# Optimization experiments

Measured on AMD Instinct MI355X. Metric: run time of the kernel, lower is better.

The kernel has to match this reference:

```python
import jax, jax.numpy as jnp
import numpy as np

B, T, DMODEL = 8, 1024, 1024
N_HEADS, DK, DV = 16, 64, 64
FF_INNER = 4096


def setup_inputs() -> dict:
    key = jax.random.key(0)
    ks = jax.random.split(key, 9)
    s = 0.02  # init scale so softmax logits stay sane
    return {
        "x": jax.random.normal(ks[0], (B, T, DMODEL), dtype=jnp.float32),
        "Wq": jax.random.normal(ks[1], (N_HEADS, DMODEL, DK), dtype=jnp.float32) * s,
        "Wk": jax.random.normal(ks[2], (N_HEADS, DMODEL, DK), dtype=jnp.float32) * s,
        "Wv": jax.random.normal(ks[3], (N_HEADS, DMODEL, DV), dtype=jnp.float32) * s,
        "Wo": jax.random.normal(ks[4], (DMODEL, DMODEL), dtype=jnp.float32) * s,
        "W1": jax.random.normal(ks[5], (FF_INNER, DMODEL), dtype=jnp.float32) * s,
        "b1": jax.random.normal(ks[6], (FF_INNER,), dtype=jnp.float32) * s,
        "W2": jax.random.normal(ks[7], (DMODEL, FF_INNER), dtype=jnp.float32) * s,
        "b2": jax.random.normal(ks[8], (DMODEL,), dtype=jnp.float32) * s,
    }


def _pseudo_norm(y):
    # Original: y - mean - std (unbiased std, torch default). NOT a real layernorm.
    mean = jnp.mean(y, axis=-1, keepdims=True)
    std = jnp.std(y, axis=-1, keepdims=True, ddof=1)
    return y - mean - std


def reference(x, Wq, Wk, Wv, Wo, W1, b1, W2, b2):
    dk = Wq.shape[-1]
    # per-head projections: (B,T,D) x (H,D,dk) -> (B,H,T,dk)
    WQ = jnp.einsum("btd,hdk->bhtk", x, Wq)
    WK = jnp.einsum("btd,hdk->bhtk", x, Wk)
    WV = jnp.einsum("btd,hdv->bhtv", x, Wv)
    scores = jnp.einsum("bhqk,bhsk->bhqs", WQ, WK) / np.sqrt(dk).astype(np.float32)
    # Faithful to original: softmax over dim=2, i.e. the QUERY axis of (B,H,Tq,Tk)
    attn = jax.nn.softmax(scores, axis=2)
    part = jnp.einsum("bhqs,bhsv->bhqv", attn, WV)  # (B,H,T,dv)
    # concat heads: (B,T,H*dv) == (B,T,dmodel)
    part = part.transpose(0, 2, 1, 3).reshape(part.shape[0], part.shape[2], -1)
    out1 = part @ Wo + x
    out1 = _pseudo_norm(out1)
    # FeedForward: Linear(dmodel->inner), relu, Linear(inner->dmodel)
    h = jnp.maximum(out1 @ W1.T + b1, 0.0)
    out2 = h @ W2.T + b2 + out1
    return _pseudo_norm(out2)
```

## Files before the change

### kernel.cpp

```cpp
#include <hip/hip_runtime.h>
#include <hip/hip_bf16.h>
#include <math.h>


#define B_ 8
#define T_ 1024
#define D_ 1024
#define H_ 16
#define DK_ 64
#define FF_ 4096
#define M_ (B_ * T_)

typedef unsigned short u16;
typedef __attribute__((ext_vector_type(8))) short bf16x8;
typedef __attribute__((ext_vector_type(4))) float f32x4;

#define QSZ 8388608ull

__device__ __forceinline__ float b2f(u16 u) {
  union { unsigned int i; float f; } x;
  x.i = ((unsigned int)u) << 16;
  return x.f;
}
__device__ __forceinline__ u16 f2b(float f) {
  __hip_bfloat16 h = __float2bfloat16(f);
  return *(u16*)&h;
}
__device__ __forceinline__ float fexp2(float x) {
#if __has_builtin(__builtin_amdgcn_exp2f)
  return __builtin_amdgcn_exp2f(x);
#else
  return exp2f(x);
#endif
}
#define C_QK 0.1803368801111244f

typedef __attribute__((address_space(1))) const void gas_void;
typedef __attribute__((address_space(3))) void las_void;
__device__ __forceinline__ void gload16(const void* g, void* l) {
  __builtin_amdgcn_global_load_lds((gas_void*)g, (las_void*)l, 16, 0, 0);
}

template <int EPI>
__global__ __launch_bounds__(256) void gemm16_k(
    const u16* __restrict__ A, const u16* __restrict__ Bt,
    int M, int N, int K, int lda, int ldb, int nbx,
    float* __restrict__ C, int ldc, u16* __restrict__ Cb,
    const float* __restrict__ res, const float* __restrict__ bias) {
  __shared__ __align__(16) u16 As[2][128 * 32];
  __shared__ __align__(16) u16 Bs[2][128 * 32];

  const int tid = threadIdx.x;
  const int lane = tid & 63, wv = tid >> 6;

  const int nwg = (int)gridDim.x;
  const int sw = (blockIdx.x & 7) * (nwg >> 3) + (blockIdx.x >> 3);
  const int m0 = (sw / nbx) * 128, n0 = (sw % nbx) * 128;

  const int wr = (wv >> 1) * 64, wc = (wv & 1) * 64;

  f32x4 acc[4][4];
#pragma unroll
  for (int i = 0; i < 4; ++i)
#pragma unroll
    for (int j = 0; j < 4; ++j) acc[i][j] = (f32x4){0.f, 0.f, 0.f, 0.f};

  const int srow = wv * 16 + (lane >> 2);
  const int scol = ((lane & 3) ^ ((lane >> 2) & 3)) * 8;
  const int fr = lane & 15, fj = lane >> 4;

  const u16* gA0 = &A[(size_t)(m0 + srow) * lda + scol];
  const u16* gA1 = &A[(size_t)(m0 + srow + 64) * lda + scol];
  const u16* gB0 = &Bt[(size_t)(n0 + srow) * ldb + scol];
  const u16* gB1 = &Bt[(size_t)(n0 + srow + 64) * ldb + scol];

  gload16(gA0, &As[0][wv * 512]);
  gload16(gA1, &As[0][2048 + wv * 512]);
  gload16(gB0, &Bs[0][wv * 512]);
  gload16(gB1, &Bs[0][2048 + wv * 512]);
  __syncthreads();

  int cur = 0;
  for (int k0 = 0; k0 < K; k0 += 32) {
    if (k0 + 32 < K) {
      int nx = cur ^ 1, ko = k0 + 32;
      gload16(gA0 + ko, &As[nx][wv * 512]);
      gload16(gA1 + ko, &As[nx][2048 + wv * 512]);
      gload16(gB0 + ko, &Bs[nx][wv * 512]);
      gload16(gB1 + ko, &Bs[nx][2048 + wv * 512]);
    }
    bf16x8 af[4], bfr[4];
#pragma unroll
    for (int mi = 0; mi < 4; ++mi) {
      int row = wr + mi * 16 + fr;
      af[mi] = *(const bf16x8*)&As[cur][row * 32 + ((fj ^ (fr & 3)) * 8)];
    }
#pragma unroll
    for (int ni = 0; ni < 4; ++ni) {
      int row = wc + ni * 16 + fr;
      bfr[ni] = *(const bf16x8*)&Bs[cur][row * 32 + ((fj ^ (fr & 3)) * 8)];
    }
#pragma unroll
    for (int mi = 0; mi < 4; ++mi)
#pragma unroll
      for (int ni = 0; ni < 4; ++ni)
        acc[mi][ni] = __builtin_amdgcn_mfma_f32_16x16x32_bf16(
            af[mi], bfr[ni], acc[mi][ni], 0, 0, 0);
    __syncthreads();
    cur ^= 1;
  }

  const int fq = (lane >> 4) * 4;
#pragma unroll
  for (int mi = 0; mi < 4; ++mi) {
#pragma unroll
    for (int ni = 0; ni < 4; ++ni) {
      const int row = m0 + wr + mi * 16 + fq;
      const int col = n0 + wc + ni * 16 + fr;
      f32x4 v = acc[mi][ni];
      if (EPI == 6) {
        const int seg = col >> 10, cl = col & 1023;
        if (seg < 2) {
          u16* dst = Cb + (size_t)seg * QSZ;
#pragma unroll
          for (int r = 0; r < 4; ++r)
            dst[(size_t)(row + r) * 1024 + cl] = f2b(v[r]);
        } else {
          ushort4 w;
          w.x = f2b(v[0]); w.y = f2b(v[1]); w.z = f2b(v[2]); w.w = f2b(v[3]);
          size_t vidx = 2 * QSZ +
                        (((size_t)(row >> 10) * 16 + (cl >> 6)) * 64 +
                         (cl & 63)) * (size_t)T_ + (row & 1023);
          *(ushort4*)&Cb[vidx] = w;
        }
      } else {
#pragma unroll
        for (int r = 0; r < 4; ++r) {
          float val = v[r];
          size_t idx = (size_t)(row + r) * ldc + col;
          if (EPI == 1) {
            C[idx] = val + res[idx];
          } else if (EPI == 2) {
            Cb[idx] = f2b(fmaxf(val + bias[col], 0.f));
          } else if (EPI == 3) {
            C[idx] = val + bias[col] + res[idx];
          }
        }
      }
    }
  }
}

__global__ __launch_bounds__(256) void cvt_k(const float* __restrict__ in,
                                             u16* __restrict__ out, int n4) {
  int i = blockIdx.x * 256 + threadIdx.x;
  if (i >= n4) return;
  float4 v = *(const float4*)&in[(size_t)i * 4];
  ushort4 o;
  o.x = f2b(v.x); o.y = f2b(v.y); o.z = f2b(v.z); o.w = f2b(v.w);
  *(ushort4*)&out[(size_t)i * 4] = o;
}

__global__ __launch_bounds__(256) void tconv_k(const float* __restrict__ src,
                                               u16* __restrict__ dst, int R,
                                               int C) {
  __shared__ __align__(16) float t[32][33];
  const size_t bo = (size_t)blockIdx.z * R * C;
  const int r0 = blockIdx.y * 32, c0 = blockIdx.x * 32;
  const int tid = threadIdx.x;
  const int row = tid >> 3, c4 = (tid & 7) * 4;
  float4 v = *(const float4*)&src[bo + (size_t)(r0 + row) * C + c0 + c4];
  t[row][c4 + 0] = v.x; t[row][c4 + 1] = v.y;
  t[row][c4 + 2] = v.z; t[row][c4 + 3] = v.w;
  __syncthreads();
  ushort4 o;
  o.x = f2b(t[c4 + 0][row]); o.y = f2b(t[c4 + 1][row]);
  o.z = f2b(t[c4 + 2][row]); o.w = f2b(t[c4 + 3][row]);
  *(ushort4*)&dst[bo + (size_t)(c0 + row) * R + r0 + c4] = o;
}

__global__ __launch_bounds__(256) void attn_lsum_k(
    const u16* __restrict__ q, const u16* __restrict__ k,
    float* __restrict__ Lrcp) {
  __shared__ __align__(16) u16 Qs[128 * 64];
  __shared__ float Lsh[2][128];
  const int tid = threadIdx.x, lane = tid & 63, wv = tid >> 6;
  const int s0 = blockIdx.x * 128, h = blockIdx.y, b = blockIdx.z;
  const int bh = b * H_ + h;
  const u16* qbase = q + (size_t)b * T_ * D_ + h * DK_;
  const u16* kbase = k + (size_t)b * T_ * D_ + h * DK_;

  const int wr = (wv >> 1) * 64, wc = (wv & 1) * 64;
  const int fr = lane & 15, fs8 = (lane >> 4) * 8, fq = (lane >> 4) * 4;

  bf16x8 kf[4][2];
#pragma unroll
  for (int mi = 0; mi < 4; ++mi)
#pragma unroll
    for (int ks = 0; ks < 2; ++ks)
      kf[mi][ks] = *(const bf16x8*)&kbase[(size_t)(s0 + wr + mi * 16 + fr) * D_ +
                                          ks * 32 + fs8];

  float lrun[4][4];
#pragma unroll
  for (int mi = 0; mi < 4; ++mi)
#pragma unroll
    for (int r = 0; r < 4; ++r) lrun[mi][r] = 0.f;

  const int srow = wv * 8 + (lane >> 3);
  const int sscol = ((lane & 7) ^ ((lane >> 3) & 7)) * 8;

  for (int q0 = 0; q0 < T_; q0 += 128) {
    __syncthreads();
#pragma unroll
    for (int it = 0; it < 4; ++it)
      gload16(&qbase[(size_t)(q0 + it * 32 + srow) * D_ + sscol],
              &Qs[(it * 32 + wv * 8) * 64]);
    __syncthreads();

    f32x4 acc[4][4];
#pragma unroll
    for (int mi = 0; mi < 4; ++mi)
#pragma unroll
      for (int ni = 0; ni < 4; ++ni) acc[mi][ni] = (f32x4){0.f, 0.f, 0.f, 0.f};

#pragma unroll
    for (int ks = 0; ks < 2; ++ks) {
      bf16x8 qf[4];
#pragma unroll
      for (int ni = 0; ni < 4; ++ni) {
        int qr = wc + ni * 16 + fr;
        int slot = (ks * 4 + (lane >> 4)) ^ (qr & 7);
        qf[ni] = *(const bf16x8*)&Qs[qr * 64 + slot * 8];
      }
#pragma unroll
      for (int mi = 0; mi < 4; ++mi)
#pragma unroll
        for (int ni = 0; ni < 4; ++ni)
          acc[mi][ni] = __builtin_amdgcn_mfma_f32_16x16x32_bf16(
              kf[mi][ks], qf[ni], acc[mi][ni], 0, 0, 0);
    }
#pragma unroll
    for (int mi = 0; mi < 4; ++mi)
#pragma unroll
      for (int r = 0; r < 4; ++r) {
        float e = 0.f;
#pragma unroll
        for (int ni = 0; ni < 4; ++ni) e += fexp2(acc[mi][ni][r] * C_QK);
        lrun[mi][r] += e;
      }
  }

#pragma unroll
  for (int mi = 0; mi < 4; ++mi)
#pragma unroll
    for (int r = 0; r < 4; ++r) {
      float s = lrun[mi][r];
      s += __shfl_xor(s, 1, 64); s += __shfl_xor(s, 2, 64);
      s += __shfl_xor(s, 4, 64); s += __shfl_xor(s, 8, 64);
      if (fr == 0) Lsh[wv & 1][wr + mi * 16 + fq + r] = s;
    }
  __syncthreads();
  if (tid < 128)
    Lrcp[(size_t)bh * T_ + s0 + tid] = 1.f / (Lsh[0][tid] + Lsh[1][tid]);
}

__global__ __launch_bounds__(256) void vscale_k(u16* __restrict__ vt,
                                                const float* __restrict__ Lrcp) {
  int i8 = blockIdx.x * 256 + threadIdx.x;
  size_t base = (size_t)i8 * 8;
  int bh = (int)(base >> 16);
  int s = (int)(base & 1023);
  float4 r0 = *(const float4*)&Lrcp[(size_t)bh * 1024 + s];
  float4 r1 = *(const float4*)&Lrcp[(size_t)bh * 1024 + s + 4];
  ushort4 a = *(const ushort4*)&vt[base];
  ushort4 c = *(const ushort4*)&vt[base + 4];
  ushort4 oa, oc;
  oa.x = f2b(b2f(a.x) * r0.x); oa.y = f2b(b2f(a.y) * r0.y);
  oa.z = f2b(b2f(a.z) * r0.z); oa.w = f2b(b2f(a.w) * r0.w);
  oc.x = f2b(b2f(c.x) * r1.x); oc.y = f2b(b2f(c.y) * r1.y);
  oc.z = f2b(b2f(c.z) * r1.z); oc.w = f2b(b2f(c.w) * r1.w);
  *(ushort4*)&vt[base] = oa;
  *(ushort4*)&vt[base + 4] = oc;
}

__global__ __launch_bounds__(256) void attn_pv_k(
    const u16* __restrict__ q, const u16* __restrict__ k,
    const u16* __restrict__ vt, u16* __restrict__ part) {
  __shared__ __align__(16) u16 Ks[128 * 64];
  __shared__ __align__(16) u16 Vs[64 * 128];
  __shared__ __align__(16) u16 Ps[128 * 128];
  const int tid = threadIdx.x, lane = tid & 63, wv = tid >> 6;
  const int q0 = blockIdx.x * 128, h = blockIdx.y, b = blockIdx.z;
  const int bh = b * H_ + h;
  const u16* qbase = q + (size_t)b * T_ * D_ + h * DK_;
  const u16* kbase = k + (size_t)b * T_ * D_ + h * DK_;
  const u16* vtb = vt + (size_t)bh * DK_ * T_;

  const int wr = (wv >> 1) * 64, wc = (wv & 1) * 64;
  const int fr = lane & 15, fs8 = (lane >> 4) * 8, fq = (lane >> 4) * 4;

  bf16x8 qf[4][2];
#pragma unroll
  for (int ni = 0; ni < 4; ++ni)
#pragma unroll
    for (int ks = 0; ks < 2; ++ks)
      qf[ni][ks] = *(const bf16x8*)&qbase[(size_t)(q0 + wc + ni * 16 + fr) * D_ +
                                          ks * 32 + fs8];

  f32x4 acc2[2][4];
#pragma unroll
  for (int i = 0; i < 2; ++i)
#pragma unroll
    for (int j = 0; j < 4; ++j) acc2[i][j] = (f32x4){0.f, 0.f, 0.f, 0.f};

  const int ksrow = wv * 8 + (lane >> 3);
  const int kscol = ((lane & 7) ^ ((lane >> 3) & 7)) * 8;

  for (int s0 = 0; s0 < T_; s0 += 128) {
    __syncthreads();
#pragma unroll
    for (int it = 0; it < 4; ++it)
      gload16(&kbase[(size_t)(s0 + it * 32 + ksrow) * D_ + kscol],
              &Ks[(it * 32 + wv * 8) * 64]);
#pragma unroll
    for (int it = 0; it < 4; ++it) {
      int v = it * 16 + wv * 4 + (lane >> 4);
      int sslot = (lane & 15) ^ (v & 7);
      gload16(&vtb[(size_t)v * T_ + s0 + sslot * 8],
              &Vs[(it * 16 + wv * 4) * 128]);
    }
    __syncthreads();

    f32x4 st[4][4];
#pragma unroll
    for (int mi = 0; mi < 4; ++mi)
#pragma unroll
      for (int ni = 0; ni < 4; ++ni) st[mi][ni] = (f32x4){0.f, 0.f, 0.f, 0.f};
#pragma unroll
    for (int ks = 0; ks < 2; ++ks) {
      bf16x8 kfa[4];
#pragma unroll
      for (int mi = 0; mi < 4; ++mi) {
        int sr = wr + mi * 16 + fr;
        int slot = (ks * 4 + (lane >> 4)) ^ (sr & 7);
        kfa[mi] = *(const bf16x8*)&Ks[sr * 64 + slot * 8];
      }
#pragma unroll
      for (int mi = 0; mi < 4; ++mi)
#pragma unroll
        for (int ni = 0; ni < 4; ++ni)
          st[mi][ni] = __builtin_amdgcn_mfma_f32_16x16x32_bf16(
              kfa[mi], qf[ni][ks], st[mi][ni], 0, 0, 0);
    }

#pragma unroll
    for (int ni = 0; ni < 4; ++ni) {
      int qcol = wc + ni * 16 + fr;
#pragma unroll
      for (int mi = 0; mi < 4; ++mi) {
        int sb = wr + mi * 16 + fq;
        u16 e0 = f2b(fexp2(st[mi][ni][0] * C_QK));
        u16 e1 = f2b(fexp2(st[mi][ni][1] * C_QK));
        u16 e2 = f2b(fexp2(st[mi][ni][2] * C_QK));
        u16 e3 = f2b(fexp2(st[mi][ni][3] * C_QK));
        uint2 w;
        w.x = (unsigned int)e0 | ((unsigned int)e1 << 16);
        w.y = (unsigned int)e2 | ((unsigned int)e3 << 16);
        int byte = qcol * 256 + ((sb * 2) ^ ((qcol & 15) << 4));
        *(uint2*)((char*)Ps + byte) = w;
      }
    }
    __syncthreads();

#pragma unroll
    for (int ks2 = 0; ks2 < 4; ++ks2) {
      bf16x8 pa[2], vb2[4];
#pragma unroll
      for (int mi2 = 0; mi2 < 2; ++mi2) {
        int qr = wv * 32 + mi2 * 16 + fr;
        int byte = qr * 256 + (((ks2 * 32 + (lane >> 4) * 8) * 2) ^ ((qr & 15) << 4));
        pa[mi2] = *(const bf16x8*)((const char*)Ps + byte);
      }
#pragma unroll
      for (int ni2 = 0; ni2 < 4; ++ni2) {
        int v = ni2 * 16 + fr;
        int slot = (ks2 * 4 + (lane >> 4)) ^ (v & 7);
        vb2[ni2] = *(const bf16x8*)&Vs[v * 128 + slot * 8];
      }
#pragma unroll
      for (int mi2 = 0; mi2 < 2; ++mi2)
#pragma unroll
        for (int ni2 = 0; ni2 < 4; ++ni2)
          acc2[mi2][ni2] = __builtin_amdgcn_mfma_f32_16x16x32_bf16(
              pa[mi2], vb2[ni2], acc2[mi2][ni2], 0, 0, 0);
    }
  }

#pragma unroll
  for (int mi2 = 0; mi2 < 2; ++mi2)
#pragma unroll
    for (int ni2 = 0; ni2 < 4; ++ni2)
#pragma unroll
      for (int r = 0; r < 4; ++r) {
        int qrow = q0 + wv * 32 + mi2 * 16 + fq + r;
        int v = ni2 * 16 + fr;
        part[(size_t)(b * T_ + qrow) * D_ + h * DK_ + v] =
            f2b(acc2[mi2][ni2][r]);
      }
}

template <bool WB>
__global__ __launch_bounds__(256) void norm_k(const float* __restrict__ in,
                                              float* __restrict__ out,
                                              u16* __restrict__ ob) {
  __shared__ float red[8];
  const int row = blockIdx.x, tid = threadIdx.x;
  float4 vv = *(const float4*)&in[(size_t)row * D_ + tid * 4];
  float s = vv.x + vv.y + vv.z + vv.w;
  for (int off = 1; off < 64; off <<= 1) s += __shfl_xor(s, off, 64);
  if ((tid & 63) == 0) red[tid >> 6] = s;
  __syncthreads();
  float mean = (red[0] + red[1] + red[2] + red[3]) * (1.f / 1024.f);
  float dx = vv.x - mean, dy = vv.y - mean, dz = vv.z - mean, dw = vv.w - mean;
  float s2 = dx * dx + dy * dy + dz * dz + dw * dw;
  __syncthreads();
  for (int off = 1; off < 64; off <<= 1) s2 += __shfl_xor(s2, off, 64);
  if ((tid & 63) == 0) red[4 + (tid >> 6)] = s2;
  __syncthreads();
  float var = (red[4] + red[5] + red[6] + red[7]) * (1.f / 1023.f);
  float sd = sqrtf(var);
  float4 o = {dx - sd, dy - sd, dz - sd, dw - sd};
  *(float4*)&out[(size_t)row * D_ + tid * 4] = o;
  if (WB) {
    ushort4 q;
    q.x = f2b(o.x); q.y = f2b(o.y); q.z = f2b(o.z); q.w = f2b(o.w);
    *(ushort4*)&ob[(size_t)row * D_ + tid * 4] = q;
  }
}

extern "C" void kernel_launch(void* const* d_in, const int* in_sizes, int n_in,
                              void* d_out, int out_size, void* d_ws,
                              size_t ws_size, hipStream_t stream) {
  const float* x  = (const float*)d_in[0];
  const float* Wq = (const float*)d_in[1];
  const float* Wk = (const float*)d_in[2];
  const float* Wv = (const float*)d_in[3];
  const float* Wo = (const float*)d_in[4];
  const float* W1 = (const float*)d_in[5];
  const float* b1 = (const float*)d_in[6];
  const float* W2 = (const float*)d_in[7];
  const float* b2 = (const float*)d_in[8];

  char* w = (char*)d_ws;
  u16* qb16   = (u16*)(w + (0ull << 20));
  u16* kb16   = (u16*)(w + (16ull << 20));
  u16* Vt     = (u16*)(w + (32ull << 20));
  u16* xb     = (u16*)(w + (48ull << 20));
  u16* part16 = (u16*)(w + (64ull << 20));
  u16* Wqkv   = (u16*)(w + (80ull << 20));
  u16* Wot    = (u16*)(w + (86ull << 20));
  u16* W1b    = (u16*)(w + (88ull << 20));
  u16* W2b    = (u16*)(w + (96ull << 20));
  float* Lrcp = (float*)(w + (104ull << 20));
  u16* o1b = qb16;
  u16* hc  = kb16;
  float* o1 = (float*)d_out;

  dim3 thr(256);

  int n4x = (M_ * D_) / 4;
  cvt_k<<<dim3((n4x + 255) / 256), thr, 0, stream>>>(x, xb, n4x);
  tconv_k<<<dim3(2, 32, 16), thr, 0, stream>>>(Wq, Wqkv, 1024, 64);
  tconv_k<<<dim3(2, 32, 16), thr, 0, stream>>>(Wk, Wqkv + 1048576, 1024, 64);
  tconv_k<<<dim3(2, 32, 16), thr, 0, stream>>>(Wv, Wqkv + 2097152, 1024, 64);
  tconv_k<<<dim3(32, 32, 1), thr, 0, stream>>>(Wo, Wot, 1024, 1024);
  int n4w = (FF_ * D_) / 4;
  cvt_k<<<dim3((n4w + 255) / 256), thr, 0, stream>>>(W1, W1b, n4w);
  cvt_k<<<dim3((n4w + 255) / 256), thr, 0, stream>>>(W2, W2b, n4w);

  gemm16_k<6><<<dim3((3072 / 128) * (M_ / 128)), thr, 0, stream>>>(
      xb, Wqkv, M_, 3072, D_, D_, D_, 3072 / 128, nullptr, D_, qb16,
      nullptr, nullptr);

  dim3 ga(T_ / 128, H_, B_);
  attn_lsum_k<<<ga, thr, 0, stream>>>(qb16, kb16, Lrcp);
  vscale_k<<<dim3((int)(QSZ / 8 / 256)), thr, 0, stream>>>(Vt, Lrcp);
  attn_pv_k<<<ga, thr, 0, stream>>>(qb16, kb16, Vt, part16);

  gemm16_k<1><<<dim3((D_ / 128) * (M_ / 128)), thr, 0, stream>>>(
      part16, Wot, M_, D_, D_, D_, D_, D_ / 128, o1, D_, nullptr, x, nullptr);
  norm_k<true><<<dim3(M_), thr, 0, stream>>>(o1, o1, o1b);

  gemm16_k<2><<<dim3((FF_ / 128) * (M_ / 128)), thr, 0, stream>>>(
      o1b, W1b, M_, FF_, D_, D_, D_, FF_ / 128, nullptr, FF_, hc,
      nullptr, b1);
  gemm16_k<3><<<dim3((D_ / 128) * (M_ / 128)), thr, 0, stream>>>(
      hc, W2b, M_, D_, FF_, FF_, FF_, D_ / 128, o1, D_, nullptr, o1, b2);

  norm_k<false><<<dim3(M_), thr, 0, stream>>>(o1, o1, nullptr);
}
```

Measured before the change: 556.3 us.

## Triple-buffer GEMM LDS tiles with explicit vmcnt waits for deeper prefetch

The bf16 MFMA GEMM moves from double to triple LDS buffering and prefetches two k-tiles ahead. Explicit s_waitcnt vmcnt counts wait only for the tile about to be consumed, and raw s_barrier plus sched_barrier replace __syncthreads. The aim is to hide more global-load latency behind MFMA work, at the cost of 50% more LDS per block, which may reduce occupancy. The hand-written waitcnt values rely on the compiler issuing no other vector memory ops inside the loop.

```diff
diff --git a/kernel.cpp b/kernel.cpp
--- a/kernel.cpp
+++ b/kernel.cpp
@@ -47,8 +47,8 @@
     int M, int N, int K, int lda, int ldb, int nbx,
     float* __restrict__ C, int ldc, u16* __restrict__ Cb,
     const float* __restrict__ res, const float* __restrict__ bias) {
-  __shared__ __align__(16) u16 As[2][128 * 32];
-  __shared__ __align__(16) u16 Bs[2][128 * 32];
+  __shared__ __align__(16) u16 As[3][128 * 32];
+  __shared__ __align__(16) u16 Bs[3][128 * 32];
 
   const int tid = threadIdx.x;
   const int lane = tid & 63, wv = tid >> 6;
@@ -74,31 +74,43 @@
   const u16* gB0 = &Bt[(size_t)(n0 + srow) * ldb + scol];
   const u16* gB1 = &Bt[(size_t)(n0 + srow + 64) * ldb + scol];
 
-  gload16(gA0, &As[0][wv * 512]);
-  gload16(gA1, &As[0][2048 + wv * 512]);
-  gload16(gB0, &Bs[0][wv * 512]);
-  gload16(gB1, &Bs[0][2048 + wv * 512]);
-  __syncthreads();
-
-  int cur = 0;
-  for (int k0 = 0; k0 < K; k0 += 32) {
-    if (k0 + 32 < K) {
-      int nx = cur ^ 1, ko = k0 + 32;
-      gload16(gA0 + ko, &As[nx][wv * 512]);
-      gload16(gA1 + ko, &As[nx][2048 + wv * 512]);
-      gload16(gB0 + ko, &Bs[nx][wv * 512]);
-      gload16(gB1 + ko, &Bs[nx][2048 + wv * 512]);
-    }
+  const int nt = K >> 5;
+#define STAGE(t, bf)                                    \
+  do {                                                  \
+    int ko_ = (t) * 32;                                 \
+    gload16(gA0 + ko_, &As[bf][wv * 512]);              \
+    gload16(gA1 + ko_, &As[bf][2048 + wv * 512]);       \
+    gload16(gB0 + ko_, &Bs[bf][wv * 512]);              \
+    gload16(gB1 + ko_, &Bs[bf][2048 + wv * 512]);       \
+  } while (0)
+
+  STAGE(0, 0);
+  STAGE(1, 1);
+
+  int bi = 0;
+  for (int t = 0; t < nt; ++t) {
+    int nx = bi + 2; if (nx >= 3) nx -= 3;
+    if (t + 2 < nt) {
+      STAGE(t + 2, nx);
+      asm volatile("s_waitcnt vmcnt(8)" ::: "memory");
+    } else if (t + 1 < nt) {
+      asm volatile("s_waitcnt vmcnt(4)" ::: "memory");
+    } else {
+      asm volatile("s_waitcnt vmcnt(0)" ::: "memory");
+    }
+    __builtin_amdgcn_s_barrier();
+    __builtin_amdgcn_sched_barrier(0);
+
     bf16x8 af[4], bfr[4];
 #pragma unroll
     for (int mi = 0; mi < 4; ++mi) {
       int row = wr + mi * 16 + fr;
-      af[mi] = *(const bf16x8*)&As[cur][row * 32 + ((fj ^ (fr & 3)) * 8)];
+      af[mi] = *(const bf16x8*)&As[bi][row * 32 + ((fj ^ (fr & 3)) * 8)];
     }
 #pragma unroll
     for (int ni = 0; ni < 4; ++ni) {
       int row = wc + ni * 16 + fr;
-      bfr[ni] = *(const bf16x8*)&Bs[cur][row * 32 + ((fj ^ (fr & 3)) * 8)];
+      bfr[ni] = *(const bf16x8*)&Bs[bi][row * 32 + ((fj ^ (fr & 3)) * 8)];
     }
 #pragma unroll
     for (int mi = 0; mi < 4; ++mi)
@@ -106,9 +118,12 @@
       for (int ni = 0; ni < 4; ++ni)
         acc[mi][ni] = __builtin_amdgcn_mfma_f32_16x16x32_bf16(
             af[mi], bfr[ni], acc[mi][ni], 0, 0, 0);
-    __syncthreads();
-    cur ^= 1;
+
+    __builtin_amdgcn_sched_barrier(0);
+    __builtin_amdgcn_s_barrier();
+    bi = (bi + 1 == 3) ? 0 : bi + 1;
   }
+#undef STAGE
 
   const int fq = (lane >> 4) * 4;
 #pragma unroll
```

Result: no change. 553.2 us (-0.5%).
